# Kernel tuning notes

Hardware: AMD Instinct MI355X
Metric: run time of the kernel (lower is better)

## Reference

```python
import jax, jax.numpy as jnp
import numpy as np

B, T_IN, T_OUT = 512, 256, 128
V, N, EH, DH, SD = 256, 1024, 64, 128, 32


def _lstm_scan(gx_seq, W_hh, h0, c0):
    """gx_seq: (T, B, 4H) precomputed input-side gates (incl. bias).
    PyTorch LSTMCell gate order: i, f, g, o."""
    def step(carry, gx):
        h, c = carry
        g = gx + h @ W_hh.T                       # (B, 4H)
        i, f, gg, o = jnp.split(g, 4, axis=-1)
        c2 = jax.nn.sigmoid(f) * c + jax.nn.sigmoid(i) * jnp.tanh(gg)
        h2 = jax.nn.sigmoid(o) * jnp.tanh(c2)
        return (h2, c2), h2
    (hT, cT), hs = jax.lax.scan(step, (h0, c0), gx_seq)
    return hT, hs


def _forward(inp_onehot, zia, tgt, fortza,
             enc_Wih, enc_Whh, enc_b, sg_W, sg_b,
             Wc_W, Wc_b, dec_Wih, dec_Whh, dec_b, out_W, out_b):
    Bb = inp_onehot.shape[0]
    dt = inp_onehot.dtype
    # ---- encoder: input projection hoisted out of the recurrence ----
    # enc_in = concat([x_t, zia]); zia is constant over t, so its gate
    # contribution is computed once (same math as the per-step cat+GEMM).
    Wx, Wz = enc_Wih[:, :V], enc_Wih[:, V:]          # (4EH,V), (4EH,N)
    gx_const = zia @ Wz.T + enc_b                    # (B, 4EH)
    gx_enc = jnp.einsum('btv,gv->tbg', inp_onehot, Wx) + gx_const[None]
    h0 = jnp.zeros((Bb, EH), dt)
    h_enc, _ = _lstm_scan(gx_enc, enc_Whh, h0, h0)   # (B, EH)
    # ---- soul update ----
    sg = jnp.concatenate([h_enc, fortza], axis=-1) @ sg_W.T + sg_b
    gate = jax.nn.sigmoid(sg[:, :SD])
    update = jnp.tanh(sg[:, SD:])
    fortza_new = gate * fortza + (1.0 - gate) * update
    # ---- decoder init ----
    dh0 = jnp.tanh(jnp.concatenate([h_enc, zia], axis=-1) @ Wc_W.T + Wc_b)
    dc0 = jnp.zeros_like(dh0)
    # ---- decoder recurrence ----
    gx_dec = jnp.einsum('btv,gv->tbg', tgt, dec_Wih) + dec_b
    _, dhs = _lstm_scan(gx_dec, dec_Whh, dh0, dc0)   # (T_out, B, DH)
    # ---- output projection: split cat([dh, fortza_new]) @ W.T ----
    Wd, Wf = out_W[:, :DH], out_W[:, DH:]
    logits = (jnp.einsum('tbh,vh->btv', dhs, Wd)
              + (fortza_new @ Wf.T)[:, None, :] + out_b)
    return logits, fortza_new


def setup_inputs() -> dict:
    key = jax.random.key(0)
    ks = jax.random.split(key, 20)
    f32 = jnp.float32
    def nrm(k, shape, s=0.05):
        return jax.random.normal(k, shape, f32) * s
    inp_idx = jax.random.randint(ks[0], (B, T_IN), 0, V)
    tgt_idx = jax.random.randint(ks[1], (B, T_OUT), 0, V)
    return {
        'inp_onehot': jax.nn.one_hot(inp_idx, V, dtype=f32),
        'zia': jax.random.uniform(ks[2], (B, N), f32),
        'tgt': jax.nn.one_hot(tgt_idx, V, dtype=f32),
        'fortza': nrm(ks[3], (B, SD), 0.5),
        'enc_Wih': nrm(ks[4], (4 * EH, V + N)),
        'enc_Whh': nrm(ks[5], (4 * EH, EH)),
        'enc_b': nrm(ks[6], (4 * EH,)),
        'sg_W': nrm(ks[7], (2 * SD, EH + SD)),
        'sg_b': nrm(ks[8], (2 * SD,)),
        'Wc_W': nrm(ks[9], (DH, EH + N)),
        'Wc_b': nrm(ks[10], (DH,)),
        'dec_Wih': nrm(ks[11], (4 * DH, V)),
        'dec_Whh': nrm(ks[12], (4 * DH, DH)),
        'dec_b': nrm(ks[13], (4 * DH,)),
        'out_W': nrm(ks[14], (V, DH + SD)),
        'out_b': nrm(ks[15], (V,)),
    }


def reference(inp_onehot, zia, tgt, fortza,
              enc_Wih, enc_Whh, enc_b, sg_W, sg_b,
              Wc_W, Wc_b, dec_Wih, dec_Whh, dec_b, out_W, out_b):
    return _forward(inp_onehot, zia, tgt, fortza,
                    enc_Wih, enc_Whh, enc_b, sg_W, sg_b,
                    Wc_W, Wc_b, dec_Wih, dec_Whh, dec_b, out_W, out_b)
```

## Files before the change

### kernel.cpp

```cpp
#include <hip/hip_runtime.h>
#include <hip/hip_bf16.h>

#define BATCH 512
#define TIN   256
#define TOUT  128
#define VOC   256
#define NZ    1024
#define EHID  64
#define DHID  128
#define SDIM  32

typedef __attribute__((ext_vector_type(8))) short bf16x8;
typedef __attribute__((ext_vector_type(4))) float f32x4;

__device__ __forceinline__ float bf2f(unsigned short u) {
  return __uint_as_float(((unsigned)u) << 16);
}
__device__ __forceinline__ unsigned short f2bf(float f) {
  unsigned u = __float_as_uint(f);
  u = u + 0x7FFFu + ((u >> 16) & 1u);
  return (unsigned short)(u >> 16);
}
__device__ __forceinline__ float sigf(float x) { return 1.0f / (1.0f + __expf(-x)); }
__device__ __forceinline__ float tanh_(float x) { return 1.0f - 2.0f / (1.0f + __expf(2.0f * x)); }

__device__ __forceinline__ bf16x8 pack8(float4 a, float4 b) {
  bf16x8 r;
  r[0] = (short)f2bf(a.x); r[1] = (short)f2bf(a.y);
  r[2] = (short)f2bf(a.z); r[3] = (short)f2bf(a.w);
  r[4] = (short)f2bf(b.x); r[5] = (short)f2bf(b.y);
  r[6] = (short)f2bf(b.z); r[7] = (short)f2bf(b.w);
  return r;
}

__global__ void k_prep(const float* __restrict__ enc_Wih, const float* __restrict__ enc_b,
                       const float* __restrict__ dec_Wih, const float* __restrict__ dec_b,
                       const float* __restrict__ out_W,
                       float* __restrict__ WxT, float* __restrict__ WdecT,
                       float* __restrict__ WdT) {
  int blk = blockIdx.x, tid = threadIdx.x;
  if (blk < 256) {
    if (tid < 256)
      WxT[blk * 256 + tid] = enc_Wih[(size_t)tid * (VOC + NZ) + blk] + enc_b[tid];
  } else if (blk < 512) {
    int v = blk - 256;
    WdecT[v * 512 + tid] = dec_Wih[(size_t)tid * VOC + v] + dec_b[tid];
  } else {
    int k = blk - 512;
    if (tid < 256)
      WdT[k * 256 + tid] = out_W[(size_t)tid * (DHID + SDIM) + k];
  }
}

__global__ void k_findidx(const float* __restrict__ src, int n_pos,
                          int* __restrict__ out) {
  int pos = blockIdx.x * 4 + (threadIdx.x >> 6);
  int lane = threadIdx.x & 63;
  if (pos >= n_pos) return;
  float4 v = ((const float4*)src)[(size_t)pos * 64 + lane];
  int comp = v.x > 0.5f ? 0 : (v.y > 0.5f ? 1 : (v.z > 0.5f ? 2 : 3));
  bool hit = (v.x > 0.5f) || (v.y > 0.5f) || (v.z > 0.5f) || (v.w > 0.5f);
  int cand = hit ? lane * 4 + comp : (1 << 30);
#pragma unroll
  for (int off = 32; off > 0; off >>= 1) {
    int o = __shfl_xor(cand, off);
    cand = cand < o ? cand : o;
  }
  if (lane == 0) out[pos] = cand < VOC ? cand : VOC - 1;
}

__global__ __launch_bounds__(256) void k_gx_const(
    const float* __restrict__ zia, const float* __restrict__ enc_Wih,
    float* __restrict__ gxc) {
  __shared__ float zs[NZ];
  int b = blockIdx.x, g = threadIdx.x;
  ((float4*)zs)[g] = ((const float4*)(zia + (size_t)b * NZ))[g];
  __syncthreads();
  float acc = 0.0f;
  const float4* wr = (const float4*)(enc_Wih + (size_t)g * (VOC + NZ) + VOC);
  const float4* z4 = (const float4*)zs;
#pragma unroll 8
  for (int k4 = 0; k4 < NZ / 4; ++k4) {
    float4 w = wr[k4], z = z4[k4];
    acc += w.x * z.x + w.y * z.y + w.z * z.z + w.w * z.w;
  }
  gxc[b * 256 + g] = acc;
}

#define ESTR 72
__global__ __launch_bounds__(256) void k_enc_scan_mfma(
    const float* __restrict__ enc_Whh, const float* __restrict__ WxT,
    const float* __restrict__ gxc, const int* __restrict__ enc_idx,
    float* __restrict__ h_enc) {
  __shared__ unsigned short hA[2][16 * ESTR];
  __shared__ int idx_s[4][TIN];
  int b0 = blockIdx.x * 4;
  int tid = threadIdx.x;
  int w = tid >> 6, lane = tid & 63, n = lane & 15, quad = lane >> 4;
  int j0 = w * 16, j = j0 + n;

  bf16x8 Bf[4][2];
#pragma unroll
  for (int ty = 0; ty < 4; ++ty)
#pragma unroll
    for (int kb = 0; kb < 2; ++kb) {
      const float* src = enc_Whh + (size_t)(ty * 64 + j0 + n) * EHID + kb * 32 + quad * 8;
      float4 x = *(const float4*)src, y = *(const float4*)(src + 4);
      Bf[ty][kb] = pack8(x, y);
    }
  for (int i = tid; i < 16 * ESTR; i += 256) { hA[0][i] = 0; hA[1][i] = 0; }
  for (int i = tid; i < 4 * TIN; i += 256)
    idx_s[i >> 8][i & 255] = enc_idx[(size_t)(b0 + (i >> 8)) * TIN + (i & 255)];
  float gc[4];
#pragma unroll
  for (int ty = 0; ty < 4; ++ty) gc[ty] = gxc[(size_t)(b0 + quad) * 256 + ty * 64 + j];
  __syncthreads();

  float gx[4];
  {
    int id0 = idx_s[quad][0];
#pragma unroll
    for (int ty = 0; ty < 4; ++ty) gx[ty] = WxT[(size_t)id0 * 256 + ty * 64 + j];
  }
  float c0 = 0.0f, h = 0.0f;
  for (int t = 0; t < TIN; ++t) {
    const unsigned short* cur = hA[t & 1];
    bf16x8 a[2];
#pragma unroll
    for (int kb = 0; kb < 2; ++kb)
      a[kb] = *(const bf16x8*)(cur + n * ESTR + kb * 32 + quad * 8);
    float gxn[4];
    int tn = (t + 1 < TIN) ? t + 1 : t;
    int idn = idx_s[quad][tn];
#pragma unroll
    for (int ty = 0; ty < 4; ++ty) gxn[ty] = WxT[(size_t)idn * 256 + ty * 64 + j];
    f32x4 acc[4];
#pragma unroll
    for (int ty = 0; ty < 4; ++ty) {
      f32x4 z; z[0] = gx[ty] + gc[ty]; z[1] = 0.f; z[2] = 0.f; z[3] = 0.f;
#pragma unroll
      for (int kb = 0; kb < 2; ++kb)
        z = __builtin_amdgcn_mfma_f32_16x16x32_bf16(a[kb], Bf[ty][kb], z, 0, 0, 0);
      acc[ty] = z;
    }
    float gi = acc[0][0], gf = acc[1][0], gg = acc[2][0], go = acc[3][0];
    c0 = sigf(gf) * c0 + sigf(gi) * tanh_(gg);
    h = sigf(go) * tanh_(c0);
    hA[(t + 1) & 1][(quad * 4) * ESTR + j] = f2bf(h);
    gx[0] = gxn[0]; gx[1] = gxn[1]; gx[2] = gxn[2]; gx[3] = gxn[3];
    __syncthreads();
  }
  h_enc[(size_t)(b0 + quad) * EHID + j] = h;
}

__global__ __launch_bounds__(256) void k_sg_fortza(
    const float* __restrict__ h_enc, const float* __restrict__ fortza,
    const float* __restrict__ sg_W, const float* __restrict__ sg_b,
    const float* __restrict__ out_W, const float* __restrict__ out_b,
    float* __restrict__ out_fortza, float* __restrict__ fout) {
  __shared__ float hf[EHID], fz[SDIM], sg_s[2 * SDIM], fn[SDIM];
  int b = blockIdx.x, tid = threadIdx.x;
  if (tid < EHID) hf[tid] = h_enc[b * EHID + tid];
  if (tid >= EHID && tid < EHID + SDIM)
    fz[tid - EHID] = fortza[(size_t)b * SDIM + (tid - EHID)];
  __syncthreads();
  if (tid < 2 * SDIM) {
    float acc = sg_b[tid];
    const float* row = sg_W + (size_t)tid * (EHID + SDIM);
    for (int k = 0; k < EHID; ++k) acc += hf[k] * row[k];
    for (int j = 0; j < SDIM; ++j) acc += fz[j] * row[EHID + j];
    sg_s[tid] = acc;
  }
  __syncthreads();
  if (tid < SDIM) {
    float gate = sigf(sg_s[tid]);
    float upd = tanh_(sg_s[SDIM + tid]);
    float v = gate * fz[tid] + (1.0f - gate) * upd;
    fn[tid] = v;
    out_fortza[(size_t)b * SDIM + tid] = v;
  }
  __syncthreads();
  {
    float acc = out_b[tid];
    const float* row = out_W + (size_t)tid * (DHID + SDIM) + DHID;
    for (int j = 0; j < SDIM; ++j) acc += fn[j] * row[j];
    fout[b * VOC + tid] = acc;
  }
}

__global__ __launch_bounds__(128) void k_dh0(
    const float* __restrict__ h_enc, const float* __restrict__ zia,
    const float* __restrict__ Wc_W, const float* __restrict__ Wc_b,
    float* __restrict__ dh0) {
  __shared__ float xs[EHID + NZ];
  int b = blockIdx.x, v = threadIdx.x;
  if (v < EHID) xs[v] = h_enc[b * EHID + v];
  for (int i = v; i < NZ / 4; i += 128)
    ((float4*)(xs + EHID))[i] = ((const float4*)(zia + (size_t)b * NZ))[i];
  __syncthreads();
  float acc = Wc_b[v];
  const float4* wr = (const float4*)(Wc_W + (size_t)v * (EHID + NZ));
  const float4* x4 = (const float4*)xs;
#pragma unroll 8
  for (int k4 = 0; k4 < (EHID + NZ) / 4; ++k4) {
    float4 w = wr[k4], x = x4[k4];
    acc += w.x * x.x + w.y * x.y + w.z * x.z + w.w * x.w;
  }
  dh0[b * DHID + v] = tanh_(acc);
}

#define DSTR 136
__global__ __launch_bounds__(512) void k_dec_scan_mfma(
    const float* __restrict__ dec_Whh, const float* __restrict__ WdecT,
    const int* __restrict__ dec_idx, const float* __restrict__ dh0,
    unsigned short* __restrict__ dhs) {
  __shared__ unsigned short hA[2][16 * DSTR];
  __shared__ int idx_s[4][TOUT];
  int b0 = blockIdx.x * 4;
  int tid = threadIdx.x;
  int w = tid >> 6, lane = tid & 63, n = lane & 15, quad = lane >> 4;
  int j0 = w * 16, j = j0 + n;

  bf16x8 Bf[4][4];
#pragma unroll
  for (int ty = 0; ty < 4; ++ty)
#pragma unroll
    for (int kb = 0; kb < 4; ++kb) {
      const float* src = dec_Whh + (size_t)(ty * 128 + j0 + n) * DHID + kb * 32 + quad * 8;
      float4 x = *(const float4*)src, y = *(const float4*)(src + 4);
      Bf[ty][kb] = pack8(x, y);
    }
  for (int i = tid; i < 16 * DSTR; i += 512) {
    int m = i / DSTR, k = i - m * DSTR;
    float v = (k < DHID && (m & 3) == 0) ? dh0[(size_t)(b0 + (m >> 2)) * DHID + k] : 0.0f;
    hA[0][i] = f2bf(v);
    hA[1][i] = 0;
  }
  for (int i = tid; i < 4 * TOUT; i += 512)
    idx_s[i >> 7][i & 127] = dec_idx[(size_t)(b0 + (i >> 7)) * TOUT + (i & 127)];
  __syncthreads();

  float gx[4];
  {
    int id0 = idx_s[quad][0];
#pragma unroll
    for (int ty = 0; ty < 4; ++ty) gx[ty] = WdecT[(size_t)id0 * 512 + ty * 128 + j];
  }
  float c0 = 0.0f;
  for (int t = 0; t < TOUT; ++t) {
    const unsigned short* cur = hA[t & 1];
    bf16x8 a[4];
#pragma unroll
    for (int kb = 0; kb < 4; ++kb)
      a[kb] = *(const bf16x8*)(cur + n * DSTR + kb * 32 + quad * 8);
    float gxn[4];
    int tn = (t + 1 < TOUT) ? t + 1 : t;
    int idn = idx_s[quad][tn];
#pragma unroll
    for (int ty = 0; ty < 4; ++ty) gxn[ty] = WdecT[(size_t)idn * 512 + ty * 128 + j];
    f32x4 acc[4];
#pragma unroll
    for (int ty = 0; ty < 4; ++ty) {
      f32x4 z; z[0] = gx[ty]; z[1] = 0.f; z[2] = 0.f; z[3] = 0.f;
#pragma unroll
      for (int kb = 0; kb < 4; ++kb)
        z = __builtin_amdgcn_mfma_f32_16x16x32_bf16(a[kb], Bf[ty][kb], z, 0, 0, 0);
      acc[ty] = z;
    }
    float gi = acc[0][0], gf = acc[1][0], gg = acc[2][0], go = acc[3][0];
    c0 = sigf(gf) * c0 + sigf(gi) * tanh_(gg);
    float h = sigf(go) * tanh_(c0);
    unsigned short hb = f2bf(h);
    hA[(t + 1) & 1][(quad * 4) * DSTR + j] = hb;
    dhs[((size_t)t * BATCH + b0 + quad) * DHID + j] = hb;
    gx[0] = gxn[0]; gx[1] = gxn[1]; gx[2] = gxn[2]; gx[3] = gxn[3];
    __syncthreads();
  }
}

__global__ __launch_bounds__(256) void k_logits(const unsigned short* __restrict__ dhs,
                                                const float* __restrict__ WdT,
                                                const float* __restrict__ fout,
                                                float* __restrict__ out) {
  __shared__ float s[DHID * 64];
  int r0 = blockIdx.x * 64;
  int t = r0 / BATCH;
  int b0 = r0 % BATCH;
  int tid = threadIdx.x;
  for (int i = tid; i < 64 * DHID; i += 256) {
    int m = i >> 7;
    int k = i & 127;
    s[k * 64 + m] = bf2f(dhs[(size_t)(r0 + m) * DHID + k]);
  }
  __syncthreads();
  int v4 = tid & 63;
  int mg = tid >> 6;
  float4 acc[16];
#pragma unroll
  for (int m = 0; m < 16; ++m) acc[m] = make_float4(0.f, 0.f, 0.f, 0.f);
  for (int k = 0; k < DHID; ++k) {
    float4 wv = ((const float4*)(WdT + k * 256))[v4];
    const float4* sk = (const float4*)(s + k * 64 + mg * 16);
#pragma unroll
    for (int j = 0; j < 4; ++j) {
      float4 h4 = sk[j];
      acc[j * 4 + 0].x += h4.x * wv.x; acc[j * 4 + 0].y += h4.x * wv.y;
      acc[j * 4 + 0].z += h4.x * wv.z; acc[j * 4 + 0].w += h4.x * wv.w;
      acc[j * 4 + 1].x += h4.y * wv.x; acc[j * 4 + 1].y += h4.y * wv.y;
      acc[j * 4 + 1].z += h4.y * wv.z; acc[j * 4 + 1].w += h4.y * wv.w;
      acc[j * 4 + 2].x += h4.z * wv.x; acc[j * 4 + 2].y += h4.z * wv.y;
      acc[j * 4 + 2].z += h4.z * wv.z; acc[j * 4 + 2].w += h4.z * wv.w;
      acc[j * 4 + 3].x += h4.w * wv.x; acc[j * 4 + 3].y += h4.w * wv.y;
      acc[j * 4 + 3].z += h4.w * wv.z; acc[j * 4 + 3].w += h4.w * wv.w;
    }
  }
#pragma unroll
  for (int m = 0; m < 16; ++m) {
    int bb = b0 + mg * 16 + m;
    float4 fo = ((const float4*)(fout + bb * VOC))[v4];
    float4 r;
    r.x = acc[m].x + fo.x;
    r.y = acc[m].y + fo.y;
    r.z = acc[m].z + fo.z;
    r.w = acc[m].w + fo.w;
    ((float4*)(out + ((size_t)bb * TOUT + t) * VOC))[v4] = r;
  }
}

extern "C" void kernel_launch(void* const* d_in, const int* in_sizes, int n_in,
                              void* d_out, int out_size, void* d_ws, size_t ws_size,
                              hipStream_t stream) {
  const float* inp_onehot = (const float*)d_in[0];
  const float* zia     = (const float*)d_in[1];
  const float* tgt     = (const float*)d_in[2];
  const float* fortza  = (const float*)d_in[3];
  const float* enc_Wih = (const float*)d_in[4];
  const float* enc_Whh = (const float*)d_in[5];
  const float* enc_b   = (const float*)d_in[6];
  const float* sg_W    = (const float*)d_in[7];
  const float* sg_b    = (const float*)d_in[8];
  const float* Wc_W    = (const float*)d_in[9];
  const float* Wc_b    = (const float*)d_in[10];
  const float* dec_Wih = (const float*)d_in[11];
  const float* dec_Whh = (const float*)d_in[12];
  const float* dec_b   = (const float*)d_in[13];
  const float* out_W   = (const float*)d_in[14];
  const float* out_b   = (const float*)d_in[15];
  float* out = (float*)d_out;

  float* ws = (float*)d_ws;
  int* enc_idx  = (int*)d_ws;
  int* dec_idx  = enc_idx + BATCH * TIN;
  float* WxT    = ws + 196608;
  float* WdecT  = ws + 262144;
  float* WdT    = ws + 393216;
  float* gxc    = ws + 425984;
  float* h_enc  = ws + 557056;
  float* dh0    = ws + 589824;
  float* fout   = ws + 655360;
  unsigned short* dhs = (unsigned short*)(ws + 786432);

  k_prep<<<640, 512, 0, stream>>>(enc_Wih, enc_b, dec_Wih, dec_b, out_W, WxT, WdecT, WdT);
  k_findidx<<<BATCH * TIN / 4, 256, 0, stream>>>(inp_onehot, BATCH * TIN, enc_idx);
  k_findidx<<<BATCH * TOUT / 4, 256, 0, stream>>>(tgt, BATCH * TOUT, dec_idx);
  k_gx_const<<<BATCH, 256, 0, stream>>>(zia, enc_Wih, gxc);
  k_enc_scan_mfma<<<BATCH / 4, 256, 0, stream>>>(enc_Whh, WxT, gxc, enc_idx, h_enc);
  k_sg_fortza<<<BATCH, 256, 0, stream>>>(h_enc, fortza, sg_W, sg_b, out_W, out_b,
                                         out + (size_t)BATCH * TOUT * VOC, fout);
  k_dh0<<<BATCH, 128, 0, stream>>>(h_enc, zia, Wc_W, Wc_b, dh0);
  k_dec_scan_mfma<<<BATCH / 4, 512, 0, stream>>>(dec_Whh, WdecT, dec_idx, dh0, dhs);
  k_logits<<<TOUT * BATCH / 64, 256, 0, stream>>>(dhs, WdT, fout, out);
}
```

Before: 629.5 us.

## Stage scan input gates in LDS chunks, tile prep transposes and small GEMMs

The encoder and decoder scans now gather several timesteps of input-gate rows into shared memory as bf16 before each chunk, instead of issuing global loads on the serial path every step. The decoder also buffers its hidden outputs in shared memory and writes them to global memory in coalesced bursts once per chunk. The weight-transpose prep kernel uses 32x32 LDS tiles, and the gx_const and dh0 projections become tiled 32x32 shared-memory GEMMs. Together these target latency on the recurrence critical path and poorly coalesced accesses. Storing input gates in bf16 adds a little extra rounding error.

```diff
diff --git a/kernel.cpp b/kernel.cpp
--- a/kernel.cpp
+++ b/kernel.cpp
@@ -33,22 +33,38 @@
   return r;
 }
 
-__global__ void k_prep(const float* __restrict__ enc_Wih, const float* __restrict__ enc_b,
-                       const float* __restrict__ dec_Wih, const float* __restrict__ dec_b,
-                       const float* __restrict__ out_W,
-                       float* __restrict__ WxT, float* __restrict__ WdecT,
-                       float* __restrict__ WdT) {
+__global__ __launch_bounds__(256) void k_prep(
+    const float* __restrict__ enc_Wih, const float* __restrict__ enc_b,
+    const float* __restrict__ dec_Wih, const float* __restrict__ dec_b,
+    const float* __restrict__ out_W,
+    float* __restrict__ WxT, float* __restrict__ WdecT, float* __restrict__ WdT) {
+  __shared__ float T[32][36];
   int blk = blockIdx.x, tid = threadIdx.x;
-  if (blk < 256) {
-    if (tid < 256)
-      WxT[blk * 256 + tid] = enc_Wih[(size_t)tid * (VOC + NZ) + blk] + enc_b[tid];
-  } else if (blk < 512) {
-    int v = blk - 256;
-    WdecT[v * 512 + tid] = dec_Wih[(size_t)tid * VOC + v] + dec_b[tid];
+  int r = tid >> 3, c = (tid & 7) * 4;
+  if (blk < 64) {
+    int g0 = (blk >> 3) * 32, v0 = (blk & 7) * 32;
+    float4 v = *(const float4*)(enc_Wih + (size_t)(g0 + r) * (VOC + NZ) + v0 + c);
+    float bias = enc_b[g0 + r];
+    T[c + 0][r] = v.x + bias; T[c + 1][r] = v.y + bias;
+    T[c + 2][r] = v.z + bias; T[c + 3][r] = v.w + bias;
+    __syncthreads();
+    *(float4*)(WxT + (size_t)(v0 + r) * 256 + g0 + c) = *(const float4*)&T[r][c];
+  } else if (blk < 192) {
+    int q = blk - 64;
+    int g0 = (q >> 3) * 32, v0 = (q & 7) * 32;
+    float4 v = *(const float4*)(dec_Wih + (size_t)(g0 + r) * VOC + v0 + c);
+    float bias = dec_b[g0 + r];
+    T[c + 0][r] = v.x + bias; T[c + 1][r] = v.y + bias;
+    T[c + 2][r] = v.z + bias; T[c + 3][r] = v.w + bias;
+    __syncthreads();
+    *(float4*)(WdecT + (size_t)(v0 + r) * 512 + g0 + c) = *(const float4*)&T[r][c];
   } else {
-    int k = blk - 512;
-    if (tid < 256)
-      WdT[k * 256 + tid] = out_W[(size_t)tid * (DHID + SDIM) + k];
+    int q = blk - 192;
+    int v0 = (q >> 2) * 32, k0 = (q & 3) * 32;
+    float4 v = *(const float4*)(out_W + (size_t)(v0 + r) * (DHID + SDIM) + k0 + c);
+    T[c + 0][r] = v.x; T[c + 1][r] = v.y; T[c + 2][r] = v.z; T[c + 3][r] = v.w;
+    __syncthreads();
+    *(float4*)(WdT + (size_t)(k0 + r) * 256 + v0 + c) = *(const float4*)&T[r][c];
   }
 }
 
@@ -72,85 +88,103 @@
 __global__ __launch_bounds__(256) void k_gx_const(
     const float* __restrict__ zia, const float* __restrict__ enc_Wih,
     float* __restrict__ gxc) {
-  __shared__ float zs[NZ];
-  int b = blockIdx.x, g = threadIdx.x;
-  ((float4*)zs)[g] = ((const float4*)(zia + (size_t)b * NZ))[g];
-  __syncthreads();
-  float acc = 0.0f;
-  const float4* wr = (const float4*)(enc_Wih + (size_t)g * (VOC + NZ) + VOC);
-  const float4* z4 = (const float4*)zs;
-#pragma unroll 8
-  for (int k4 = 0; k4 < NZ / 4; ++k4) {
-    float4 w = wr[k4], z = z4[k4];
-    acc += w.x * z.x + w.y * z.y + w.z * z.z + w.w * z.w;
-  }
-  gxc[b * 256 + g] = acc;
+  __shared__ float As[32][36], Bs[32][36];
+  int b0 = blockIdx.x * 32, g0 = blockIdx.y * 32;
+  int tid = threadIdx.x;
+  int ldr = tid >> 3, ldc = (tid & 7) * 4;
+  int tx = tid & 15, ty = tid >> 4;
+  float a00 = 0.f, a01 = 0.f, a10 = 0.f, a11 = 0.f;
+  for (int kc = 0; kc < NZ; kc += 32) {
+    float4 av = *(const float4*)(zia + (size_t)(b0 + ldr) * NZ + kc + ldc);
+    float4 bv = *(const float4*)(enc_Wih + (size_t)(g0 + ldr) * (VOC + NZ) + VOC + kc + ldc);
+    __syncthreads();
+    As[ldc + 0][ldr] = av.x; As[ldc + 1][ldr] = av.y;
+    As[ldc + 2][ldr] = av.z; As[ldc + 3][ldr] = av.w;
+    Bs[ldc + 0][ldr] = bv.x; Bs[ldc + 1][ldr] = bv.y;
+    Bs[ldc + 2][ldr] = bv.z; Bs[ldc + 3][ldr] = bv.w;
+    __syncthreads();
+#pragma unroll
+    for (int k = 0; k < 32; ++k) {
+      float x0 = As[k][tx * 2], x1 = As[k][tx * 2 + 1];
+      float y0 = Bs[k][ty * 2], y1 = Bs[k][ty * 2 + 1];
+      a00 += x0 * y0; a01 += x0 * y1; a10 += x1 * y0; a11 += x1 * y1;
+    }
+  }
+  float* o = gxc + (size_t)(b0 + tx * 2) * 256 + g0 + ty * 2;
+  o[0] = a00; o[1] = a01; o[256] = a10; o[257] = a11;
 }
 
 #define ESTR 72
-__global__ __launch_bounds__(256) void k_enc_scan_mfma(
+#define ECH  16
+__global__ __launch_bounds__(256) void k_enc_scan(
     const float* __restrict__ enc_Whh, const float* __restrict__ WxT,
     const float* __restrict__ gxc, const int* __restrict__ enc_idx,
     float* __restrict__ h_enc) {
   __shared__ unsigned short hA[2][16 * ESTR];
-  __shared__ int idx_s[4][TIN];
-  int b0 = blockIdx.x * 4;
-  int tid = threadIdx.x;
-  int w = tid >> 6, lane = tid & 63, n = lane & 15, quad = lane >> 4;
-  int j0 = w * 16, j = j0 + n;
+  __shared__ unsigned short gxs[ECH * 4 * 256];
+  __shared__ int idx_s[4 * TIN];
+  int b0 = blockIdx.x * 4, tid = threadIdx.x;
+  int w = tid >> 6, lane = tid & 63, n = lane & 15, q = lane >> 4;
+  int j = w * 16 + n;
 
   bf16x8 Bf[4][2];
 #pragma unroll
   for (int ty = 0; ty < 4; ++ty)
 #pragma unroll
     for (int kb = 0; kb < 2; ++kb) {
-      const float* src = enc_Whh + (size_t)(ty * 64 + j0 + n) * EHID + kb * 32 + quad * 8;
-      float4 x = *(const float4*)src, y = *(const float4*)(src + 4);
-      Bf[ty][kb] = pack8(x, y);
-    }
+      const float* s = enc_Whh + (size_t)(ty * 64 + j) * EHID + kb * 32 + q * 8;
+      Bf[ty][kb] = pack8(*(const float4*)s, *(const float4*)(s + 4));
+    }
+  float gc[4];
+#pragma unroll
+  for (int ty = 0; ty < 4; ++ty) gc[ty] = gxc[(size_t)(b0 + q) * 256 + ty * 64 + j];
   for (int i = tid; i < 16 * ESTR; i += 256) { hA[0][i] = 0; hA[1][i] = 0; }
   for (int i = tid; i < 4 * TIN; i += 256)
-    idx_s[i >> 8][i & 255] = enc_idx[(size_t)(b0 + (i >> 8)) * TIN + (i & 255)];
-  float gc[4];
-#pragma unroll
-  for (int ty = 0; ty < 4; ++ty) gc[ty] = gxc[(size_t)(b0 + quad) * 256 + ty * 64 + j];
-  __syncthreads();
-
-  float gx[4];
-  {
-    int id0 = idx_s[quad][0];
-#pragma unroll
-    for (int ty = 0; ty < 4; ++ty) gx[ty] = WxT[(size_t)id0 * 256 + ty * 64 + j];
-  }
-  float c0 = 0.0f, h = 0.0f;
-  for (int t = 0; t < TIN; ++t) {
-    const unsigned short* cur = hA[t & 1];
-    bf16x8 a[2];
-#pragma unroll
-    for (int kb = 0; kb < 2; ++kb)
-      a[kb] = *(const bf16x8*)(cur + n * ESTR + kb * 32 + quad * 8);
-    float gxn[4];
-    int tn = (t + 1 < TIN) ? t + 1 : t;
-    int idn = idx_s[quad][tn];
-#pragma unroll
-    for (int ty = 0; ty < 4; ++ty) gxn[ty] = WxT[(size_t)idn * 256 + ty * 64 + j];
-    f32x4 acc[4];
-#pragma unroll
-    for (int ty = 0; ty < 4; ++ty) {
-      f32x4 z; z[0] = gx[ty] + gc[ty]; z[1] = 0.f; z[2] = 0.f; z[3] = 0.f;
+    idx_s[i] = enc_idx[(size_t)(b0 + (i >> 8)) * TIN + (i & 255)];
+  __syncthreads();
+
+  float c0 = 0.f, h = 0.f;
+  for (int tc = 0; tc < TIN; tc += ECH) {
+    for (int rr = 0; rr < 16; ++rr) {
+      int rowid = w * 16 + rr;
+      int tt = rowid >> 2, b = rowid & 3;
+      int idx = idx_s[b * TIN + tc + tt];
+      float4 v = *(const float4*)(WxT + (size_t)idx * 256 + lane * 4);
+      unsigned short* dst = gxs + ((tt * 4 + b) << 8);
+      int g0 = lane * 4;
+      int ty = g0 >> 6;
+      dst[((g0 + 0) & 63) * 4 + ty] = f2bf(v.x);
+      dst[((g0 + 1) & 63) * 4 + ty] = f2bf(v.y);
+      dst[((g0 + 2) & 63) * 4 + ty] = f2bf(v.z);
+      dst[((g0 + 3) & 63) * 4 + ty] = f2bf(v.w);
+    }
+    __syncthreads();
+    for (int tt = 0; tt < ECH; ++tt) {
+      int t = tc + tt;
+      const unsigned short* cur = hA[t & 1];
+      bf16x8 a[2];
 #pragma unroll
       for (int kb = 0; kb < 2; ++kb)
-        z = __builtin_amdgcn_mfma_f32_16x16x32_bf16(a[kb], Bf[ty][kb], z, 0, 0, 0);
-      acc[ty] = z;
-    }
-    float gi = acc[0][0], gf = acc[1][0], gg = acc[2][0], go = acc[3][0];
-    c0 = sigf(gf) * c0 + sigf(gi) * tanh_(gg);
-    h = sigf(go) * tanh_(c0);
-    hA[(t + 1) & 1][(quad * 4) * ESTR + j] = f2bf(h);
-    gx[0] = gxn[0]; gx[1] = gxn[1]; gx[2] = gxn[2]; gx[3] = gxn[3];
-    __syncthreads();
-  }
-  h_enc[(size_t)(b0 + quad) * EHID + j] = h;
+        a[kb] = *(const bf16x8*)(cur + n * ESTR + kb * 32 + q * 8);
+      ushort4 gx4 = *(const ushort4*)(gxs + ((tt * 4 + q) << 8) + j * 4);
+      f32x4 zz[4];
+#pragma unroll
+      for (int ty = 0; ty < 4; ++ty) {
+        f32x4 z;
+        z[0] = bf2f(((const unsigned short*)&gx4)[ty]) + gc[ty];
+        z[1] = 0.f; z[2] = 0.f; z[3] = 0.f;
+        z = __builtin_amdgcn_mfma_f32_16x16x32_bf16(a[0], Bf[ty][0], z, 0, 0, 0);
+        z = __builtin_amdgcn_mfma_f32_16x16x32_bf16(a[1], Bf[ty][1], z, 0, 0, 0);
+        zz[ty] = z;
+      }
+      float gi = zz[0][0], gf = zz[1][0], gg = zz[2][0], go = zz[3][0];
+      c0 = sigf(gf) * c0 + sigf(gi) * tanh_(gg);
+      h = sigf(go) * tanh_(c0);
+      hA[(t + 1) & 1][(q * 4) * ESTR + j] = f2bf(h);
+      __syncthreads();
+    }
+  }
+  h_enc[(size_t)(b0 + q) * EHID + j] = h;
 }
 
 __global__ __launch_bounds__(256) void k_sg_fortza(
@@ -168,7 +202,7 @@
     float acc = sg_b[tid];
     const float* row = sg_W + (size_t)tid * (EHID + SDIM);
     for (int k = 0; k < EHID; ++k) acc += hf[k] * row[k];
-    for (int j = 0; j < SDIM; ++j) acc += fz[j] * row[EHID + j];
+    for (int jj = 0; jj < SDIM; ++jj) acc += fz[jj] * row[EHID + jj];
     sg_s[tid] = acc;
   }
   __syncthreads();
@@ -183,98 +217,146 @@
   {
     float acc = out_b[tid];
     const float* row = out_W + (size_t)tid * (DHID + SDIM) + DHID;
-    for (int j = 0; j < SDIM; ++j) acc += fn[j] * row[j];
+    for (int jj = 0; jj < SDIM; ++jj) acc += fn[jj] * row[jj];
     fout[b * VOC + tid] = acc;
   }
 }
 
-__global__ __launch_bounds__(128) void k_dh0(
+__global__ __launch_bounds__(256) void k_dh0(
     const float* __restrict__ h_enc, const float* __restrict__ zia,
     const float* __restrict__ Wc_W, const float* __restrict__ Wc_b,
     float* __restrict__ dh0) {
-  __shared__ float xs[EHID + NZ];
-  int b = blockIdx.x, v = threadIdx.x;
-  if (v < EHID) xs[v] = h_enc[b * EHID + v];
-  for (int i = v; i < NZ / 4; i += 128)
-    ((float4*)(xs + EHID))[i] = ((const float4*)(zia + (size_t)b * NZ))[i];
-  __syncthreads();
-  float acc = Wc_b[v];
-  const float4* wr = (const float4*)(Wc_W + (size_t)v * (EHID + NZ));
-  const float4* x4 = (const float4*)xs;
-#pragma unroll 8
-  for (int k4 = 0; k4 < (EHID + NZ) / 4; ++k4) {
-    float4 w = wr[k4], x = x4[k4];
-    acc += w.x * x.x + w.y * x.y + w.z * x.z + w.w * x.w;
-  }
-  dh0[b * DHID + v] = tanh_(acc);
+  __shared__ float As[32][36], Bs[32][36];
+  int b0 = blockIdx.x * 32, v0 = blockIdx.y * 32;
+  int tid = threadIdx.x;
+  int ldr = tid >> 3, ldc = (tid & 7) * 4;
+  int tx = tid & 15, ty = tid >> 4;
+  float a00 = 0.f, a01 = 0.f, a10 = 0.f, a11 = 0.f;
+  for (int kc = 0; kc < EHID + NZ; kc += 32) {
+    float4 av;
+    if (kc < EHID)
+      av = *(const float4*)(h_enc + (size_t)(b0 + ldr) * EHID + kc + ldc);
+    else
+      av = *(const float4*)(zia + (size_t)(b0 + ldr) * NZ + (kc - EHID) + ldc);
+    float4 bv = *(const float4*)(Wc_W + (size_t)(v0 + ldr) * (EHID + NZ) + kc + ldc);
+    __syncthreads();
+    As[ldc + 0][ldr] = av.x; As[ldc + 1][ldr] = av.y;
+    As[ldc + 2][ldr] = av.z; As[ldc + 3][ldr] = av.w;
+    Bs[ldc + 0][ldr] = bv.x; Bs[ldc + 1][ldr] = bv.y;
+    Bs[ldc + 2][ldr] = bv.z; Bs[ldc + 3][ldr] = bv.w;
+    __syncthreads();
+#pragma unroll
+    for (int k = 0; k < 32; ++k) {
+      float x0 = As[k][tx * 2], x1 = As[k][tx * 2 + 1];
+      float y0 = Bs[k][ty * 2], y1 = Bs[k][ty * 2 + 1];
+      a00 += x0 * y0; a01 += x0 * y1; a10 += x1 * y0; a11 += x1 * y1;
+    }
+  }
+  float bb0 = Wc_b[v0 + ty * 2], bb1 = Wc_b[v0 + ty * 2 + 1];
+  float* o = dh0 + (size_t)(b0 + tx * 2) * DHID + v0 + ty * 2;
+  o[0] = tanh_(a00 + bb0); o[1] = tanh_(a01 + bb1);
+  o[DHID] = tanh_(a10 + bb0); o[DHID + 1] = tanh_(a11 + bb1);
 }
 
 #define DSTR 136
-__global__ __launch_bounds__(512) void k_dec_scan_mfma(
+#define DCH  8
+__global__ __launch_bounds__(512) void k_dec_scan(
     const float* __restrict__ dec_Whh, const float* __restrict__ WdecT,
     const int* __restrict__ dec_idx, const float* __restrict__ dh0,
     unsigned short* __restrict__ dhs) {
   __shared__ unsigned short hA[2][16 * DSTR];
-  __shared__ int idx_s[4][TOUT];
-  int b0 = blockIdx.x * 4;
-  int tid = threadIdx.x;
-  int w = tid >> 6, lane = tid & 63, n = lane & 15, quad = lane >> 4;
-  int j0 = w * 16, j = j0 + n;
+  __shared__ unsigned short gxs[DCH * 4 * 512];
+  __shared__ unsigned short hH[DCH * 4 * DHID];
+  __shared__ int idx_s[4 * TOUT];
+  int b0 = blockIdx.x * 4, tid = threadIdx.x;
+  int w = tid >> 6, lane = tid & 63, n = lane & 15, q = lane >> 4;
+  int j = w * 16 + n;
 
   bf16x8 Bf[4][4];
 #pragma unroll
   for (int ty = 0; ty < 4; ++ty)
 #pragma unroll
     for (int kb = 0; kb < 4; ++kb) {
-      const float* src = dec_Whh + (size_t)(ty * 128 + j0 + n) * DHID + kb * 32 + quad * 8;
-      float4 x = *(const float4*)src, y = *(const float4*)(src + 4);
-      Bf[ty][kb] = pack8(x, y);
+      const float* s = dec_Whh + (size_t)(ty * 128 + j) * DHID + kb * 32 + q * 8;
+      Bf[ty][kb] = pack8(*(const float4*)s, *(const float4*)(s + 4));
     }
   for (int i = tid; i < 16 * DSTR; i += 512) {
     int m = i / DSTR, k = i - m * DSTR;
-    float v = (k < DHID && (m & 3) == 0) ? dh0[(size_t)(b0 + (m >> 2)) * DHID + k] : 0.0f;
+    float v = (k < DHID && (m & 3) == 0) ? dh0[(size_t)(b0 + (m >> 2)) * DHID + k] : 0.f;
     hA[0][i] = f2bf(v);
     hA[1][i] = 0;
   }
   for (int i = tid; i < 4 * TOUT; i += 512)
-    idx_s[i >> 7][i & 127] = dec_idx[(size_t)(b0 + (i >> 7)) * TOUT + (i & 127)];
-  __syncthreads();
-
-  float gx[4];
+    idx_s[i] = dec_idx[(size_t)(b0 + (i >> 7)) * TOUT + (i & 127)];
+  __syncthreads();
+
+  float c0 = 0.f;
+  for (int tc = 0; tc < TOUT; tc += DCH) {
+    if (tc > 0) {
+      int tp = tc - DCH;
+      for (int u = tid; u < DCH * 4 * DHID / 4; u += 512) {
+        int jj = (u & 31) * 4;
+        int rowid = u >> 5;
+        int tt = rowid >> 2, b = rowid & 3;
+        *(ushort4*)(dhs + ((size_t)(tp + tt) * BATCH + (b0 + b)) * DHID + jj) =
+            *(const ushort4*)(hH + (rowid << 7) + jj);
+      }
+    }
+    for (int rr = 0; rr < 4; ++rr) {
+      int rowid = w * 4 + rr;
+      int tt = rowid >> 2, b = rowid & 3;
+      int idx = idx_s[b * TOUT + tc + tt];
+      const float* srow = WdecT + (size_t)idx * 512;
+      unsigned short* dst = gxs + ((tt * 4 + b) << 9);
+#pragma unroll
+      for (int hs = 0; hs < 2; ++hs) {
+        float4 v = *(const float4*)(srow + hs * 256 + lane * 4);
+        int g0 = hs * 256 + lane * 4;
+        int ty = g0 >> 7;
+        dst[((g0 + 0) & 127) * 4 + ty] = f2bf(v.x);
+        dst[((g0 + 1) & 127) * 4 + ty] = f2bf(v.y);
+        dst[((g0 + 2) & 127) * 4 + ty] = f2bf(v.z);
+        dst[((g0 + 3) & 127) * 4 + ty] = f2bf(v.w);
+      }
+    }
+    __syncthreads();
+    for (int tt = 0; tt < DCH; ++tt) {
+      int t = tc + tt;
+      const unsigned short* cur = hA[t & 1];
+      bf16x8 a[4];
+#pragma unroll
+      for (int kb = 0; kb < 4; ++kb)
+        a[kb] = *(const bf16x8*)(cur + n * DSTR + kb * 32 + q * 8);
+      ushort4 gx4 = *(const ushort4*)(gxs + ((tt * 4 + q) << 9) + j * 4);
+      f32x4 zz[4];
+#pragma unroll
+      for (int ty = 0; ty < 4; ++ty) {
+        f32x4 z;
+        z[0] = bf2f(((const unsigned short*)&gx4)[ty]);
+        z[1] = 0.f; z[2] = 0.f; z[3] = 0.f;
+#pragma unroll
+        for (int kb = 0; kb < 4; ++kb)
+          z = __builtin_amdgcn_mfma_f32_16x16x32_bf16(a[kb], Bf[ty][kb], z, 0, 0, 0);
+        zz[ty] = z;
+      }
+      float gi = zz[0][0], gf = zz[1][0], gg = zz[2][0], go = zz[3][0];
+      c0 = sigf(gf) * c0 + sigf(gi) * tanh_(gg);
+      float h = sigf(go) * tanh_(c0);
+      unsigned short hb = f2bf(h);
+      hA[(t + 1) & 1][(q * 4) * DSTR + j] = hb;
+      hH[((tt * 4 + q) << 7) + j] = hb;
+      __syncthreads();
+    }
+  }
   {
-    int id0 = idx_s[quad][0];
-#pragma unroll
-    for (int ty = 0; ty < 4; ++ty) gx[ty] = WdecT[(size_t)id0 * 512 + ty * 128 + j];
-  }
-  float c0 = 0.0f;
-  for (int t = 0; t < TOUT; ++t) {
-    const unsigned short* cur = hA[t & 1];
-    bf16x8 a[4];
-#pragma unroll
-    for (int kb = 0; kb < 4; ++kb)
-      a[kb] = *(const bf16x8*)(cur + n * DSTR + kb * 32 + quad * 8);
-    float gxn[4];
-    int tn = (t + 1 < TOUT) ? t + 1 : t;
-    int idn = idx_s[quad][tn];
-#pragma unroll
-    for (int ty = 0; ty < 4; ++ty) gxn[ty] = WdecT[(size_t)idn * 512 + ty * 128 + j];
-    f32x4 acc[4];
-#pragma unroll
-    for (int ty = 0; ty < 4; ++ty) {
-      f32x4 z; z[0] = gx[ty]; z[1] = 0.f; z[2] = 0.f; z[3] = 0.f;
-#pragma unroll
-      for (int kb = 0; kb < 4; ++kb)
-        z = __builtin_amdgcn_mfma_f32_16x16x32_bf16(a[kb], Bf[ty][kb], z, 0, 0, 0);
-      acc[ty] = z;
-    }
-    float gi = acc[0][0], gf = acc[1][0], gg = acc[2][0], go = acc[3][0];
-    c0 = sigf(gf) * c0 + sigf(gi) * tanh_(gg);
-    float h = sigf(go) * tanh_(c0);
-    unsigned short hb = f2bf(h);
-    hA[(t + 1) & 1][(quad * 4) * DSTR + j] = hb;
-    dhs[((size_t)t * BATCH + b0 + quad) * DHID + j] = hb;
-    gx[0] = gxn[0]; gx[1] = gxn[1]; gx[2] = gxn[2]; gx[3] = gxn[3];
-    __syncthreads();
+    int tp = TOUT - DCH;
+    for (int u = tid; u < DCH * 4 * DHID / 4; u += 512) {
+      int jj = (u & 31) * 4;
+      int rowid = u >> 5;
+      int tt = rowid >> 2, b = rowid & 3;
+      *(ushort4*)(dhs + ((size_t)(tp + tt) * BATCH + (b0 + b)) * DHID + jj) =
+          *(const ushort4*)(hH + (rowid << 7) + jj);
+    }
   }
 }
 
@@ -302,16 +384,16 @@
     float4 wv = ((const float4*)(WdT + k * 256))[v4];
     const float4* sk = (const float4*)(s + k * 64 + mg * 16);
 #pragma unroll
-    for (int j = 0; j < 4; ++j) {
-      float4 h4 = sk[j];
-      acc[j * 4 + 0].x += h4.x * wv.x; acc[j * 4 + 0].y += h4.x * wv.y;
-      acc[j * 4 + 0].z += h4.x * wv.z; acc[j * 4 + 0].w += h4.x * wv.w;
-      acc[j * 4 + 1].x += h4.y * wv.x; acc[j * 4 + 1].y += h4.y * wv.y;
-      acc[j * 4 + 1].z += h4.y * wv.z; acc[j * 4 + 1].w += h4.y * wv.w;
-      acc[j * 4 + 2].x += h4.z * wv.x; acc[j * 4 + 2].y += h4.z * wv.y;
-      acc[j * 4 + 2].z += h4.z * wv.z; acc[j * 4 + 2].w += h4.z * wv.w;
-      acc[j * 4 + 3].x += h4.w * wv.x; acc[j * 4 + 3].y += h4.w * wv.y;
-      acc[j * 4 + 3].z += h4.w * wv.z; acc[j * 4 + 3].w += h4.w * wv.w;
+    for (int jj = 0; jj < 4; ++jj) {
+      float4 h4 = sk[jj];
+      acc[jj * 4 + 0].x += h4.x * wv.x; acc[jj * 4 + 0].y += h4.x * wv.y;
+      acc[jj * 4 + 0].z += h4.x * wv.z; acc[jj * 4 + 0].w += h4.x * wv.w;
+      acc[jj * 4 + 1].x += h4.y * wv.x; acc[jj * 4 + 1].y += h4.y * wv.y;
+      acc[jj * 4 + 1].z += h4.y * wv.z; acc[jj * 4 + 1].w += h4.y * wv.w;
+      acc[jj * 4 + 2].x += h4.z * wv.x; acc[jj * 4 + 2].y += h4.z * wv.y;
+      acc[jj * 4 + 2].z += h4.z * wv.z; acc[jj * 4 + 2].w += h4.z * wv.w;
+      acc[jj * 4 + 3].x += h4.w * wv.x; acc[jj * 4 + 3].y += h4.w * wv.y;
+      acc[jj * 4 + 3].z += h4.w * wv.z; acc[jj * 4 + 3].w += h4.w * wv.w;
     }
   }
 #pragma unroll
@@ -360,14 +442,14 @@
   float* fout   = ws + 655360;
   unsigned short* dhs = (unsigned short*)(ws + 786432);
 
-  k_prep<<<640, 512, 0, stream>>>(enc_Wih, enc_b, dec_Wih, dec_b, out_W, WxT, WdecT, WdT);
+  k_prep<<<224, 256, 0, stream>>>(enc_Wih, enc_b, dec_Wih, dec_b, out_W, WxT, WdecT, WdT);
   k_findidx<<<BATCH * TIN / 4, 256, 0, stream>>>(inp_onehot, BATCH * TIN, enc_idx);
   k_findidx<<<BATCH * TOUT / 4, 256, 0, stream>>>(tgt, BATCH * TOUT, dec_idx);
-  k_gx_const<<<BATCH, 256, 0, stream>>>(zia, enc_Wih, gxc);
-  k_enc_scan_mfma<<<BATCH / 4, 256, 0, stream>>>(enc_Whh, WxT, gxc, enc_idx, h_enc);
+  k_gx_const<<<dim3(16, 8), 256, 0, stream>>>(zia, enc_Wih, gxc);
+  k_enc_scan<<<BATCH / 4, 256, 0, stream>>>(enc_Whh, WxT, gxc, enc_idx, h_enc);
   k_sg_fortza<<<BATCH, 256, 0, stream>>>(h_enc, fortza, sg_W, sg_b, out_W, out_b,
                                          out + (size_t)BATCH * TOUT * VOC, fout);
-  k_dh0<<<BATCH, 128, 0, stream>>>(h_enc, zia, Wc_W, Wc_b, dh0);
-  k_dec_scan_mfma<<<BATCH / 4, 512, 0, stream>>>(dec_Whh, WdecT, dec_idx, dh0, dhs);
+  k_dh0<<<dim3(16, 4), 256, 0, stream>>>(h_enc, zia, Wc_W, Wc_b, dh0);
+  k_dec_scan<<<BATCH / 4, 512, 0, stream>>>(dec_Whh, WdecT, dec_idx, dh0, dhs);
   k_logits<<<TOUT * BATCH / 64, 256, 0, stream>>>(dhs, WdT, fout, out);
 }
```

Measured after the change: 684.7 us. 1.09x slower.
